# Kernel tuning notes

Hardware: AMD Instinct MI355X
Metric: run time of the kernel (lower is better)

## Reference

```python
import jax, jax.numpy as jnp
import numpy as np

B, V = 256, 5000          # batch, num variables
C, S = 20000, 3           # num cliques, clique size
NC = 2 ** S               # number of binary combinations per clique


def setup_inputs() -> dict:
    key = jax.random.key(0)
    k1, k2, k3 = jax.random.split(key, 3)
    x = jax.random.uniform(k1, (B, V), dtype=jnp.float32)
    # exact bit enumeration as in precompute(): row j = bits of j, MSB first
    binary_combinations = jnp.array(
        [[(j >> k) & 1 for k in range(S - 1, -1, -1)] for j in range(NC)],
        dtype=jnp.float32,
    )
    all_vars = jax.random.randint(k2, (C, S), 0, V, dtype=jnp.int32)
    all_factors = jax.random.normal(k3, (C, NC), dtype=jnp.float32)
    return {
        "x": x,
        "binary_combinations": binary_combinations,
        "all_vars": all_vars,
        "all_factors": all_factors,
    }


def reference(x, binary_combinations, all_vars, all_factors):
    # gather clique variable values: [B, C, S]
    all_values = x[:, all_vars.reshape(-1)].reshape(x.shape[0], C, S)
    # match against each binary combination: [B, NC, C, S]
    av = all_values[:, None, :, :]            # [B,1,C,S]
    bc = binary_combinations[None, :, None, :]  # [1,NC,1,S]
    selected = av * bc + (1.0 - av) * (1.0 - bc)
    # product over clique members -> [B, NC, C]
    product_term = jnp.prod(selected, axis=3)
    # weight by factor tables (all_factors.T broadcast) and reduce over combos -> [B, C]
    scores = jnp.sum(product_term * all_factors.T[None, :, :], axis=1)
    # total log-score per example (evaluate_parallel_clique_dict) -> [B]
    ll_scores = jnp.sum(scores, axis=1)
    return ll_scores
```

## Files before the change

### kernel.cpp

```cpp
#include <hip/hip_runtime.h>

#define BATCH 256
#define NV    5000
#define NCLS  20000
#define G     4
#define NT    512
#define NCH   8

__device__ __forceinline__ float eval4(float f0, float d0, float f2, float d1,
                                       float f4, float d2, float f6, float d3,
                                       float p0, float p1, float p2) {
    float t0 = fmaf(d0, p2, f0);
    float t1 = fmaf(d1, p2, f2);
    float t2 = fmaf(d2, p2, f4);
    float t3 = fmaf(d3, p2, f6);
    float u0 = fmaf(t1 - t0, p1, t0);
    float u1 = fmaf(t3 - t2, p1, t2);
    return fmaf(u1 - u0, p0, u0);
}

__global__ __launch_bounds__(NT)
void bmn_main(const float* __restrict__ x,
              const int*   __restrict__ vars,
              const float* __restrict__ factors,
              float* __restrict__ outbuf,
              int cchunk) {
    __shared__ float xs[NV * G];
    const int bg  = blockIdx.x;
    const int cs  = blockIdx.y;
    const int tid = threadIdx.x;

    const float* xr = x + bg * G * NV;
    for (int i = tid; i < NV; i += NT) {
        float4 v;
        v.x = xr[i];
        v.y = xr[i + NV];
        v.z = xr[i + 2 * NV];
        v.w = xr[i + 3 * NV];
        *reinterpret_cast<float4*>(&xs[i * 4]) = v;
    }
    __syncthreads();

    float4 acc = make_float4(0.f, 0.f, 0.f, 0.f);
    const int cbase = cs * cchunk;
    const int cend  = cbase + cchunk;
    for (int c = cbase + tid; c < cend; c += NT) {
        const int v0 = vars[c * 3 + 0];
        const int v1 = vars[c * 3 + 1];
        const int v2 = vars[c * 3 + 2];
        const float4 fa = *reinterpret_cast<const float4*>(factors + c * 8);
        const float4 fb = *reinterpret_cast<const float4*>(factors + c * 8 + 4);
        const float4 p0 = *reinterpret_cast<const float4*>(&xs[v0 * 4]);
        const float4 p1 = *reinterpret_cast<const float4*>(&xs[v1 * 4]);
        const float4 p2 = *reinterpret_cast<const float4*>(&xs[v2 * 4]);
        const float d0 = fa.y - fa.x, d1 = fa.w - fa.z;
        const float d2 = fb.y - fb.x, d3 = fb.w - fb.z;
        acc.x += eval4(fa.x, d0, fa.z, d1, fb.x, d2, fb.z, d3, p0.x, p1.x, p2.x);
        acc.y += eval4(fa.x, d0, fa.z, d1, fb.x, d2, fb.z, d3, p0.y, p1.y, p2.y);
        acc.z += eval4(fa.x, d0, fa.z, d1, fb.x, d2, fb.z, d3, p0.z, p1.z, p2.z);
        acc.w += eval4(fa.x, d0, fa.z, d1, fb.x, d2, fb.z, d3, p0.w, p1.w, p2.w);
    }

    for (int off = 32; off; off >>= 1) {
        acc.x += __shfl_down(acc.x, off, 64);
        acc.y += __shfl_down(acc.y, off, 64);
        acc.z += __shfl_down(acc.z, off, 64);
        acc.w += __shfl_down(acc.w, off, 64);
    }
    __shared__ float red[NT / 64][G];
    if ((tid & 63) == 0) {
        const int w = tid >> 6;
        red[w][0] = acc.x; red[w][1] = acc.y; red[w][2] = acc.z; red[w][3] = acc.w;
    }
    __syncthreads();
    if (tid < G) {
        float s = 0.f;
        #pragma unroll
        for (int w = 0; w < NT / 64; ++w) s += red[w][tid];
        outbuf[cs * BATCH + bg * G + tid] = s;
    }
}

__global__ __launch_bounds__(BATCH)
void bmn_reduce(const float* __restrict__ ws, float* __restrict__ out) {
    const int b = threadIdx.x;
    float s = 0.f;
    #pragma unroll
    for (int cs = 0; cs < NCH; ++cs) s += ws[cs * BATCH + b];
    out[b] = s;
}

extern "C" void kernel_launch(void* const* d_in, const int* in_sizes, int n_in,
                              void* d_out, int out_size, void* d_ws, size_t ws_size,
                              hipStream_t stream) {
    const float* x       = (const float*)d_in[0];
    const int*   vars    = (const int*)d_in[2];
    const float* factors = (const float*)d_in[3];
    float* out = (float*)d_out;

    if (ws_size >= (size_t)(NCH * BATCH) * sizeof(float)) {
        float* ws = (float*)d_ws;
        bmn_main<<<dim3(BATCH / G, NCH), NT, 0, stream>>>(x, vars, factors, ws, NCLS / NCH);
        bmn_reduce<<<1, BATCH, 0, stream>>>(ws, out);
    } else {
        bmn_main<<<dim3(BATCH / G, 1), NT, 0, stream>>>(x, vars, factors, out, NCLS);
    }
}
```

Before: 12.44 us.

## Transpose x to variable-major layout and parallelize over clique chunks

Adds a tiled transpose kernel that writes x as [V, B] in workspace. The main kernel then assigns one block per 20-clique chunk with one thread per batch row, so gathers of a variable read coalesced batch vectors from global/L2 instead of each block staging a 4-row slice of x in shared memory. Per-chunk partials go to a 1000x256 buffer, which a new multi-block reduce sums. This removes the redundant per-block shared-memory staging of x, at the cost of an extra transpose pass, a third launch and a larger partial-sum buffer.

```diff
diff --git a/kernel.cpp b/kernel.cpp
--- a/kernel.cpp
+++ b/kernel.cpp
@@ -1,15 +1,35 @@
 #include <hip/hip_runtime.h>
 
-#define BATCH 256
-#define NV    5000
-#define NCLS  20000
-#define G     4
-#define NT    512
-#define NCH   8
+#define BATCH  256
+#define NV     5000
+#define NCLS   20000
+#define NCHUNK 1000
+#define CHUNK  20
+#define TB     64
 
-__device__ __forceinline__ float eval4(float f0, float d0, float f2, float d1,
-                                       float f4, float d2, float f6, float d3,
-                                       float p0, float p1, float p2) {
+__global__ __launch_bounds__(256)
+void bmn_transpose(const float* __restrict__ x, float* __restrict__ xT) {
+    __shared__ float tile[TB][TB + 1];
+    const int v0 = blockIdx.x * TB;
+    const int b0 = blockIdx.y * TB;
+    const int tx = threadIdx.x & 63;
+    const int ty = threadIdx.x >> 6;
+    #pragma unroll
+    for (int j = 0; j < TB; j += 4) {
+        const int v = v0 + tx;
+        tile[j + ty][tx] = (v < NV) ? x[(b0 + j + ty) * NV + v] : 0.f;
+    }
+    __syncthreads();
+    #pragma unroll
+    for (int j = 0; j < TB; j += 4) {
+        const int v = v0 + j + ty;
+        if (v < NV) xT[v * BATCH + b0 + tx] = tile[tx][j + ty];
+    }
+}
+
+__device__ __forceinline__ float eval_c(float f0, float d0, float f2, float d1,
+                                        float f4, float d2, float f6, float d3,
+                                        float p0, float p1, float p2) {
     float t0 = fmaf(d0, p2, f0);
     float t1 = fmaf(d1, p2, f2);
     float t2 = fmaf(d2, p2, f4);
@@ -19,75 +39,73 @@
     return fmaf(u1 - u0, p0, u0);
 }
 
-__global__ __launch_bounds__(NT)
-void bmn_main(const float* __restrict__ x,
+__global__ __launch_bounds__(256)
+void bmn_main(const float* __restrict__ xT,
               const int*   __restrict__ vars,
               const float* __restrict__ factors,
-              float* __restrict__ outbuf,
-              int cchunk) {
-    __shared__ float xs[NV * G];
-    const int bg  = blockIdx.x;
-    const int cs  = blockIdx.y;
-    const int tid = threadIdx.x;
-
-    const float* xr = x + bg * G * NV;
-    for (int i = tid; i < NV; i += NT) {
-        float4 v;
-        v.x = xr[i];
-        v.y = xr[i + NV];
-        v.z = xr[i + 2 * NV];
-        v.w = xr[i + 3 * NV];
-        *reinterpret_cast<float4*>(&xs[i * 4]) = v;
-    }
-    __syncthreads();
-
-    float4 acc = make_float4(0.f, 0.f, 0.f, 0.f);
-    const int cbase = cs * cchunk;
-    const int cend  = cbase + cchunk;
-    for (int c = cbase + tid; c < cend; c += NT) {
+              float* __restrict__ partial) {
+    const int cs = blockIdx.x;
+    const int b  = threadIdx.x;
+    const int cbase = cs * CHUNK;
+    float acc = 0.f;
+    #pragma unroll 4
+    for (int k = 0; k < CHUNK; ++k) {
+        const int c = cbase + k;
         const int v0 = vars[c * 3 + 0];
         const int v1 = vars[c * 3 + 1];
         const int v2 = vars[c * 3 + 2];
         const float4 fa = *reinterpret_cast<const float4*>(factors + c * 8);
         const float4 fb = *reinterpret_cast<const float4*>(factors + c * 8 + 4);
-        const float4 p0 = *reinterpret_cast<const float4*>(&xs[v0 * 4]);
-        const float4 p1 = *reinterpret_cast<const float4*>(&xs[v1 * 4]);
-        const float4 p2 = *reinterpret_cast<const float4*>(&xs[v2 * 4]);
+        const float p0 = xT[v0 * BATCH + b];
+        const float p1 = xT[v1 * BATCH + b];
+        const float p2 = xT[v2 * BATCH + b];
         const float d0 = fa.y - fa.x, d1 = fa.w - fa.z;
         const float d2 = fb.y - fb.x, d3 = fb.w - fb.z;
-        acc.x += eval4(fa.x, d0, fa.z, d1, fb.x, d2, fb.z, d3, p0.x, p1.x, p2.x);
-        acc.y += eval4(fa.x, d0, fa.z, d1, fb.x, d2, fb.z, d3, p0.y, p1.y, p2.y);
-        acc.z += eval4(fa.x, d0, fa.z, d1, fb.x, d2, fb.z, d3, p0.z, p1.z, p2.z);
-        acc.w += eval4(fa.x, d0, fa.z, d1, fb.x, d2, fb.z, d3, p0.w, p1.w, p2.w);
+        acc += eval_c(fa.x, d0, fa.z, d1, fb.x, d2, fb.z, d3, p0, p1, p2);
     }
-
-    for (int off = 32; off; off >>= 1) {
-        acc.x += __shfl_down(acc.x, off, 64);
-        acc.y += __shfl_down(acc.y, off, 64);
-        acc.z += __shfl_down(acc.z, off, 64);
-        acc.w += __shfl_down(acc.w, off, 64);
-    }
-    __shared__ float red[NT / 64][G];
-    if ((tid & 63) == 0) {
-        const int w = tid >> 6;
-        red[w][0] = acc.x; red[w][1] = acc.y; red[w][2] = acc.z; red[w][3] = acc.w;
-    }
-    __syncthreads();
-    if (tid < G) {
-        float s = 0.f;
-        #pragma unroll
-        for (int w = 0; w < NT / 64; ++w) s += red[w][tid];
-        outbuf[cs * BATCH + bg * G + tid] = s;
-    }
+    partial[cs * BATCH + b] = acc;
 }
 
-__global__ __launch_bounds__(BATCH)
-void bmn_reduce(const float* __restrict__ ws, float* __restrict__ out) {
-    const int b = threadIdx.x;
+__global__ __launch_bounds__(256)
+void bmn_reduce(const float* __restrict__ partial, float* __restrict__ out) {
+    const int b = blockIdx.x;
+    const int t = threadIdx.x;
     float s = 0.f;
-    #pragma unroll
-    for (int cs = 0; cs < NCH; ++cs) s += ws[cs * BATCH + b];
-    out[b] = s;
+    for (int cs = t; cs < NCHUNK; cs += 256)
+        s += partial[cs * BATCH + b];
+    for (int off = 32; off; off >>= 1)
+        s += __shfl_down(s, off, 64);
+    __shared__ float red[4];
+    if ((t & 63) == 0) red[t >> 6] = s;
+    __syncthreads();
+    if (t == 0) out[b] = red[0] + red[1] + red[2] + red[3];
+}
+
+__global__ __launch_bounds__(256)
+void bmn_fallback(const float* __restrict__ x,
+                  const int*   __restrict__ vars,
+                  const float* __restrict__ factors,
+                  float* __restrict__ out) {
+    const int b = blockIdx.x;
+    const int t = threadIdx.x;
+    const float* xb = x + b * NV;
+    float acc = 0.f;
+    for (int c = t; c < NCLS; c += 256) {
+        const int v0 = vars[c * 3 + 0];
+        const int v1 = vars[c * 3 + 1];
+        const int v2 = vars[c * 3 + 2];
+        const float4 fa = *reinterpret_cast<const float4*>(factors + c * 8);
+        const float4 fb = *reinterpret_cast<const float4*>(factors + c * 8 + 4);
+        const float d0 = fa.y - fa.x, d1 = fa.w - fa.z;
+        const float d2 = fb.y - fb.x, d3 = fb.w - fb.z;
+        acc += eval_c(fa.x, d0, fa.z, d1, fb.x, d2, fb.z, d3, xb[v0], xb[v1], xb[v2]);
+    }
+    for (int off = 32; off; off >>= 1)
+        acc += __shfl_down(acc, off, 64);
+    __shared__ float red[4];
+    if ((t & 63) == 0) red[t >> 6] = acc;
+    __syncthreads();
+    if (t == 0) out[b] = red[0] + red[1] + red[2] + red[3];
 }
 
 extern "C" void kernel_launch(void* const* d_in, const int* in_sizes, int n_in,
@@ -98,11 +116,15 @@
     const float* factors = (const float*)d_in[3];
     float* out = (float*)d_out;
 
-    if (ws_size >= (size_t)(NCH * BATCH) * sizeof(float)) {
-        float* ws = (float*)d_ws;
-        bmn_main<<<dim3(BATCH / G, NCH), NT, 0, stream>>>(x, vars, factors, ws, NCLS / NCH);
-        bmn_reduce<<<1, BATCH, 0, stream>>>(ws, out);
+    const size_t xt_elems = (size_t)NV * BATCH;
+    const size_t pp_elems = (size_t)NCHUNK * BATCH;
+    if (ws_size >= (xt_elems + pp_elems) * sizeof(float)) {
+        float* xT      = (float*)d_ws;
+        float* partial = xT + xt_elems;
+        bmn_transpose<<<dim3((NV + TB - 1) / TB, BATCH / TB), 256, 0, stream>>>(x, xT);
+        bmn_main<<<NCHUNK, 256, 0, stream>>>(xT, vars, factors, partial);
+        bmn_reduce<<<BATCH, 256, 0, stream>>>(partial, out);
     } else {
-        bmn_main<<<dim3(BATCH / G, 1), NT, 0, stream>>>(x, vars, factors, out, NCLS);
+        bmn_fallback<<<BATCH, 256, 0, stream>>>(x, vars, factors, out);
     }
 }
```

Measured after the change: 25.53 us. 2.05x slower.

## Prefetch clique data into registers before x staging; replace reduce kernel with atomics

Applied to the files above, without the earlier changes.

The kernel now issues all per-thread loads of clique indices and factor tables into registers before the shared-memory staging of x. This lets those global loads overlap the x copy, and the clique loop is fully unrolled over a fixed count with a masked tail. The separate reduction kernel is replaced by a memset plus atomicAdd of each block's partial sums into the output, and launch bounds now request higher occupancy. In exchange, register pressure rises, and the atomic accumulation makes the order of the float additions nondeterministic.

```diff
diff --git a/kernel.cpp b/kernel.cpp
--- a/kernel.cpp
+++ b/kernel.cpp
@@ -6,10 +6,13 @@
 #define G     4
 #define NT    512
 #define NCH   8
+#define CCH   (NCLS / NCH)
+#define NBLK  (NCH * BATCH / G)
+#define KMAX  5
 
-__device__ __forceinline__ float eval4(float f0, float d0, float f2, float d1,
-                                       float f4, float d2, float f6, float d3,
-                                       float p0, float p1, float p2) {
+__device__ __forceinline__ float eval_c(float f0, float d0, float f2, float d1,
+                                        float f4, float d2, float f6, float d3,
+                                        float p0, float p1, float p2) {
     float t0 = fmaf(d0, p2, f0);
     float t1 = fmaf(d1, p2, f2);
     float t2 = fmaf(d2, p2, f4);
@@ -19,16 +22,35 @@
     return fmaf(u1 - u0, p0, u0);
 }
 
-__global__ __launch_bounds__(NT)
+__global__ __launch_bounds__(NT, 4)
 void bmn_main(const float* __restrict__ x,
               const int*   __restrict__ vars,
               const float* __restrict__ factors,
-              float* __restrict__ outbuf,
-              int cchunk) {
+              float* __restrict__ out) {
     __shared__ float xs[NV * G];
-    const int bg  = blockIdx.x;
-    const int cs  = blockIdx.y;
+    const int bg  = blockIdx.x & (BATCH / G - 1);
+    const int cs  = blockIdx.x >> 6;
     const int tid = threadIdx.x;
+    const int cbase = cs * CCH;
+    const int c0    = cbase + tid;
+
+    int   va[KMAX], vb[KMAX], vc[KMAX];
+    float4 FA[KMAX], FB[KMAX];
+    #pragma unroll
+    for (int k = 0; k < KMAX; ++k) {
+        int c = c0 + k * NT;
+        if (k == KMAX - 1 && c >= cbase + CCH) c = c0;
+        va[k] = vars[c * 3 + 0];
+        vb[k] = vars[c * 3 + 1];
+        vc[k] = vars[c * 3 + 2];
+        FA[k] = *reinterpret_cast<const float4*>(factors + c * 8);
+        FB[k] = *reinterpret_cast<const float4*>(factors + c * 8 + 4);
+    }
+    {
+        const float m = (c0 + (KMAX - 1) * NT < cbase + CCH) ? 1.f : 0.f;
+        FA[KMAX - 1].x *= m; FA[KMAX - 1].y *= m; FA[KMAX - 1].z *= m; FA[KMAX - 1].w *= m;
+        FB[KMAX - 1].x *= m; FB[KMAX - 1].y *= m; FB[KMAX - 1].z *= m; FB[KMAX - 1].w *= m;
+    }
 
     const float* xr = x + bg * G * NV;
     for (int i = tid; i < NV; i += NT) {
@@ -41,24 +63,19 @@
     }
     __syncthreads();
 
+    const float4* xs4 = reinterpret_cast<const float4*>(xs);
     float4 acc = make_float4(0.f, 0.f, 0.f, 0.f);
-    const int cbase = cs * cchunk;
-    const int cend  = cbase + cchunk;
-    for (int c = cbase + tid; c < cend; c += NT) {
-        const int v0 = vars[c * 3 + 0];
-        const int v1 = vars[c * 3 + 1];
-        const int v2 = vars[c * 3 + 2];
-        const float4 fa = *reinterpret_cast<const float4*>(factors + c * 8);
-        const float4 fb = *reinterpret_cast<const float4*>(factors + c * 8 + 4);
-        const float4 p0 = *reinterpret_cast<const float4*>(&xs[v0 * 4]);
-        const float4 p1 = *reinterpret_cast<const float4*>(&xs[v1 * 4]);
-        const float4 p2 = *reinterpret_cast<const float4*>(&xs[v2 * 4]);
-        const float d0 = fa.y - fa.x, d1 = fa.w - fa.z;
-        const float d2 = fb.y - fb.x, d3 = fb.w - fb.z;
-        acc.x += eval4(fa.x, d0, fa.z, d1, fb.x, d2, fb.z, d3, p0.x, p1.x, p2.x);
-        acc.y += eval4(fa.x, d0, fa.z, d1, fb.x, d2, fb.z, d3, p0.y, p1.y, p2.y);
-        acc.z += eval4(fa.x, d0, fa.z, d1, fb.x, d2, fb.z, d3, p0.z, p1.z, p2.z);
-        acc.w += eval4(fa.x, d0, fa.z, d1, fb.x, d2, fb.z, d3, p0.w, p1.w, p2.w);
+    #pragma unroll
+    for (int k = 0; k < KMAX; ++k) {
+        const float4 p0 = xs4[va[k]];
+        const float4 p1 = xs4[vb[k]];
+        const float4 p2 = xs4[vc[k]];
+        const float d0 = FA[k].y - FA[k].x, d1 = FA[k].w - FA[k].z;
+        const float d2 = FB[k].y - FB[k].x, d3 = FB[k].w - FB[k].z;
+        acc.x += eval_c(FA[k].x, d0, FA[k].z, d1, FB[k].x, d2, FB[k].z, d3, p0.x, p1.x, p2.x);
+        acc.y += eval_c(FA[k].x, d0, FA[k].z, d1, FB[k].x, d2, FB[k].z, d3, p0.y, p1.y, p2.y);
+        acc.z += eval_c(FA[k].x, d0, FA[k].z, d1, FB[k].x, d2, FB[k].z, d3, p0.z, p1.z, p2.z);
+        acc.w += eval_c(FA[k].x, d0, FA[k].z, d1, FB[k].x, d2, FB[k].z, d3, p0.w, p1.w, p2.w);
     }
 
     for (int off = 32; off; off >>= 1) {
@@ -77,17 +94,8 @@
         float s = 0.f;
         #pragma unroll
         for (int w = 0; w < NT / 64; ++w) s += red[w][tid];
-        outbuf[cs * BATCH + bg * G + tid] = s;
+        atomicAdd(&out[bg * G + tid], s);
     }
-}
-
-__global__ __launch_bounds__(BATCH)
-void bmn_reduce(const float* __restrict__ ws, float* __restrict__ out) {
-    const int b = threadIdx.x;
-    float s = 0.f;
-    #pragma unroll
-    for (int cs = 0; cs < NCH; ++cs) s += ws[cs * BATCH + b];
-    out[b] = s;
 }
 
 extern "C" void kernel_launch(void* const* d_in, const int* in_sizes, int n_in,
@@ -98,11 +106,6 @@
     const float* factors = (const float*)d_in[3];
     float* out = (float*)d_out;
 
-    if (ws_size >= (size_t)(NCH * BATCH) * sizeof(float)) {
-        float* ws = (float*)d_ws;
-        bmn_main<<<dim3(BATCH / G, NCH), NT, 0, stream>>>(x, vars, factors, ws, NCLS / NCH);
-        bmn_reduce<<<1, BATCH, 0, stream>>>(ws, out);
-    } else {
-        bmn_main<<<dim3(BATCH / G, 1), NT, 0, stream>>>(x, vars, factors, out, NCLS);
-    }
+    hipMemsetAsync(out, 0, (size_t)BATCH * sizeof(float), stream);
+    bmn_main<<<dim3(NBLK), NT, 0, stream>>>(x, vars, factors, out);
 }
```

New measurement: 16.54 us. +33.0%, slower.
